# Performance work log

Measured on AMD Instinct MI355X. Metric: run time of the kernel, lower is better.

The kernel has to match this reference:

```python
import jax, jax.numpy as jnp
from jax import lax
import numpy as np

H, W = 240, 304
IN_CH, OUT_CH, K = 16, 32, 3
B = 8
N_PER = 65536
N = B * N_PER
CIN = IN_CH + 2  # pos + neg + features


def setup_inputs() -> dict:
    key = jax.random.key(0)
    k1, k2, k3, k4, k5 = jax.random.split(key, 5)
    # events columns: x, y, t in [0,1); polarity in {0,1}
    xyt = jax.random.uniform(k1, (N, 3), dtype=jnp.float32)
    pol = jax.random.randint(k2, (N, 1), 0, 2).astype(jnp.float32)
    events = jnp.concatenate([xyt, pol], axis=1)
    features = jax.random.normal(k3, (N, IN_CH), dtype=jnp.float32)
    offsets = (jnp.arange(1, B + 1, dtype=jnp.int64) * N_PER)  # cumulative counts
    # SubmanifoldConvolution params: one [CIN, OUT_CH] matrix per filter offset -> HWIO
    fan_in = K * K * CIN
    weight = jax.random.normal(k4, (K, K, CIN, OUT_CH), dtype=jnp.float32) / np.sqrt(fan_in)
    bias = jax.random.normal(k5, (OUT_CH,), dtype=jnp.float32) * 0.01
    return {"events": events, "features": features, "weight": weight,
            "bias": bias, "offsets": offsets}


def reference(events, features, weight, bias, offsets):
    n = events.shape[0]
    b = offsets.shape[0]
    # offset2batch: row i belongs to first sample whose cumulative offset exceeds i
    batch = jnp.searchsorted(offsets, jnp.arange(n, dtype=offsets.dtype), side="right").astype(jnp.int32)
    pos = events[:, 3:4]
    neg = 1.0 - pos
    sparse = jnp.concatenate([pos, neg, features], axis=1)  # [N, CIN]
    # yx = events[:, [1, 0]] scaled by (h, w), rounded to grid coords
    yi = jnp.clip(jnp.round(events[:, 1] * H).astype(jnp.int32), 0, H - 1)
    xi = jnp.clip(jnp.round(events[:, 0] * W).astype(jnp.int32), 0, W - 1)
    key = (batch * H + yi) * W + xi  # linear site id, [N]
    nseg = b * H * W
    # scn InputLayer mode=4: average features of duplicate coordinates
    feat_sum = jax.ops.segment_sum(sparse, key, num_segments=nseg)  # [nseg, CIN]
    cnt = jax.ops.segment_sum(jnp.ones((n,), sparse.dtype), key, num_segments=nseg)
    dense = feat_sum / jnp.maximum(cnt, 1.0)[:, None]
    dense = dense.reshape(b, H, W, CIN)  # zeros at inactive sites
    # Submanifold 3x3 conv: inactive neighbors are zero, so a dense SAME conv
    # evaluated only at active sites matches the submanifold rulebook math.
    out = lax.conv_general_dilated(dense, weight, window_strides=(1, 1),
                                   padding="SAME",
                                   dimension_numbers=("NHWC", "HWIO", "NHWC"))
    out = out.reshape(nseg, OUT_CH)
    # OutputLayer: read back per input row (active sites only), add bias there
    f = out[key] + bias  # [N, OUT_CH]
    return f
```

## Files before the change

kernel.cpp:

```cpp
#include <hip/hip_runtime.h>

#define Hh 240
#define Ww 304
#define IN_CH 16
#define OUT_CH 32
#define Bb 8
#define N_PER 65536
#define N_EV (Bb * N_PER)
#define CIN (IN_CH + 2)
#define NSEG (Bb * Hh * Ww)
#define NBLK 570

#define TW 32
#define TH 8
#define HW_ 34
#define HH_ 10
#define NXT_TILES 10
#define NYT_TILES 30
#define OPITCH 33

typedef __attribute__((ext_vector_type(8))) short bf16x8;
typedef __attribute__((ext_vector_type(4))) float f32x4;

__device__ __forceinline__ unsigned short f2bf(float x) {
  unsigned u = __float_as_uint(x);
  unsigned r = u + 0x7fffu + ((u >> 16) & 1u);
  return (unsigned short)(r >> 16);
}
__device__ __forceinline__ float bf2f(unsigned short b) {
  return __uint_as_float(((unsigned)b) << 16);
}

__global__ __launch_bounds__(256) void hist_rank_kernel(
    const float* __restrict__ events, const int* __restrict__ offsets,
    int* __restrict__ hist, int* __restrict__ keyArr, int* __restrict__ rankArr) {
  int i = blockIdx.x * blockDim.x + threadIdx.x;
  float4 ev = ((const float4*)events)[i];
  int yi = (int)rintf(ev.y * (float)Hh);
  yi = min(max(yi, 0), Hh - 1);
  int xi = (int)rintf(ev.x * (float)Ww);
  xi = min(max(xi, 0), Ww - 1);
  int b = 0;
#pragma unroll
  for (int j = 0; j < Bb; j++) b += (offsets[j] <= i) ? 1 : 0;
  int key = (b * Hh + yi) * Ww + xi;
  int pol = (ev.w != 0.0f) ? 1 : 0;
  keyArr[i] = key | (pol << 31);
  rankArr[i] = atomicAdd(&hist[key], 1);
}

__global__ __launch_bounds__(256) void scan1_kernel(
    const int* __restrict__ hist, int* __restrict__ baseLocal,
    int* __restrict__ blockSum) {
  __shared__ int lds[256];
  int b = blockIdx.x, t = threadIdx.x;
  int idx = b * 1024 + t * 4;
  int4 v = *(const int4*)(hist + idx);
  int s0 = v.x, s1 = s0 + v.y, s2 = s1 + v.z, s3 = s2 + v.w;
  lds[t] = s3;
  __syncthreads();
  int val = s3;
  for (int off = 1; off < 256; off <<= 1) {
    int n = (t >= off) ? lds[t - off] : 0;
    __syncthreads();
    val += n;
    lds[t] = val;
    __syncthreads();
  }
  int excl = val - s3;
  int4 o;
  o.x = excl; o.y = excl + s0; o.z = excl + s1; o.w = excl + s2;
  *(int4*)(baseLocal + idx) = o;
  if (t == 255) blockSum[b] = val;
}

__global__ __launch_bounds__(1024) void scan2_kernel(
    const int* __restrict__ blockSum, int* __restrict__ blockOffset) {
  __shared__ int lds[1024];
  int t = threadIdx.x;
  int v = (t < NBLK) ? blockSum[t] : 0;
  lds[t] = v;
  __syncthreads();
  int val = v;
  for (int off = 1; off < 1024; off <<= 1) {
    int n = (t >= off) ? lds[t - off] : 0;
    __syncthreads();
    val += n;
    lds[t] = val;
    __syncthreads();
  }
  if (t < NBLK) blockOffset[t] = val - v;
  if (t == 0) blockOffset[NBLK] = lds[1023];
}

__global__ __launch_bounds__(256) void prep_weights_kernel(
    const float* __restrict__ weight, unsigned short* __restrict__ wprep) {
  int tid = threadIdx.x;
#pragma unroll
  for (int it = 0; it < 24; it++) {
    int idx = it * 256 + tid;
    int ky = idx >> 11;
    int rem = idx & 2047;
    int n = rem >> 6;
    int kl = rem & 63;
    unsigned short v = 0;
    if (kl < 54) {
      int kx = kl / 18, ci = kl - kx * 18;
      v = f2bf(weight[((ky * 3 + kx) * CIN + ci) * OUT_CH + n]);
    }
    wprep[idx] = v;
  }
}

__global__ __launch_bounds__(256) void scatter_feat_kernel(
    const float* __restrict__ features, const int* __restrict__ keyArr,
    const int* __restrict__ rankArr, const int* __restrict__ baseLocal,
    const int* __restrict__ blockOffset, uint4* __restrict__ sortedFeat,
    int* __restrict__ sortedMeta) {
  int i = blockIdx.x * blockDim.x + threadIdx.x;
  int meta = keyArr[i];
  int key = meta & 0x7fffffff;
  int pos = baseLocal[key] + blockOffset[key >> 10] + rankArr[i];
  const float4* f = (const float4*)(features + (size_t)i * IN_CH);
  float4 f0 = f[0], f1 = f[1], f2 = f[2], f3 = f[3];
  uint4 w0, w1;
  w0.x = (unsigned)f2bf(f0.x) | ((unsigned)f2bf(f0.y) << 16);
  w0.y = (unsigned)f2bf(f0.z) | ((unsigned)f2bf(f0.w) << 16);
  w0.z = (unsigned)f2bf(f1.x) | ((unsigned)f2bf(f1.y) << 16);
  w0.w = (unsigned)f2bf(f1.z) | ((unsigned)f2bf(f1.w) << 16);
  w1.x = (unsigned)f2bf(f2.x) | ((unsigned)f2bf(f2.y) << 16);
  w1.y = (unsigned)f2bf(f2.z) | ((unsigned)f2bf(f2.w) << 16);
  w1.z = (unsigned)f2bf(f3.x) | ((unsigned)f2bf(f3.y) << 16);
  w1.w = (unsigned)f2bf(f3.z) | ((unsigned)f2bf(f3.w) << 16);
  sortedFeat[(size_t)pos * 2] = w0;
  sortedFeat[(size_t)pos * 2 + 1] = w1;
  sortedMeta[pos] = i | (meta & 0x80000000);
}

__global__ __launch_bounds__(256) void fused_conv_kernel(
    const uint4* __restrict__ sortedFeat, const int* __restrict__ sortedMeta,
    const int* __restrict__ baseLocal, const int* __restrict__ blockOffset,
    const unsigned short* __restrict__ wprep, const float* __restrict__ bias,
    float* __restrict__ out) {
  __shared__ unsigned smem[128 * OPITCH];
  __shared__ int ibase[TH * TW];
  __shared__ int icnt[TH * TW];

  int blk = blockIdx.x;
  int xt = blk % NXT_TILES;
  int rem = blk / NXT_TILES;
  int yt = rem % NYT_TILES;
  int b = rem / NYT_TILES;
  int x0 = xt * TW, y0 = yt * TH;
  int tid = threadIdx.x;

  if (tid < 12) smem[3060 + tid] = 0;

  for (int h = tid; h < HH_ * HW_; h += 256) {
    int hy = h / HW_, hx = h % HW_;
    int gy = y0 - 1 + hy, gx = x0 - 1 + hx;
    float acc[CIN];
#pragma unroll
    for (int k = 0; k < CIN; k++) acc[k] = 0.0f;
    int c = 0, base = 0;
    if (gy >= 0 && gy < Hh && gx >= 0 && gx < Ww) {
      int p = (b * Hh + gy) * Ww + gx;
      int bo = blockOffset[p >> 10];
      base = baseLocal[p] + bo;
      int nxt = ((p & 1023) != 1023) ? (baseLocal[p + 1] + bo)
                                     : blockOffset[(p >> 10) + 1];
      c = nxt - base;
      for (int j = 0; j < c; j++) {
        int e = sortedMeta[base + j];
        float pol = (float)((unsigned)e >> 31);
        acc[0] += pol;
        acc[1] += 1.0f - pol;
        uint4 w0 = sortedFeat[(size_t)(base + j) * 2];
        uint4 w1 = sortedFeat[(size_t)(base + j) * 2 + 1];
        acc[2] += bf2f((unsigned short)w0.x);  acc[3] += bf2f((unsigned short)(w0.x >> 16));
        acc[4] += bf2f((unsigned short)w0.y);  acc[5] += bf2f((unsigned short)(w0.y >> 16));
        acc[6] += bf2f((unsigned short)w0.z);  acc[7] += bf2f((unsigned short)(w0.z >> 16));
        acc[8] += bf2f((unsigned short)w0.w);  acc[9] += bf2f((unsigned short)(w0.w >> 16));
        acc[10] += bf2f((unsigned short)w1.x); acc[11] += bf2f((unsigned short)(w1.x >> 16));
        acc[12] += bf2f((unsigned short)w1.y); acc[13] += bf2f((unsigned short)(w1.y >> 16));
        acc[14] += bf2f((unsigned short)w1.z); acc[15] += bf2f((unsigned short)(w1.z >> 16));
        acc[16] += bf2f((unsigned short)w1.w); acc[17] += bf2f((unsigned short)(w1.w >> 16));
      }
    }
    float inv = 1.0f / fmaxf((float)c, 1.0f);
    unsigned* row = smem + 9 * h;
#pragma unroll
    for (int k = 0; k < 9; k++)
      row[k] = (unsigned)f2bf(acc[2 * k] * inv) |
               ((unsigned)f2bf(acc[2 * k + 1] * inv) << 16);
    if (hx >= 1 && hx <= TW && hy >= 1 && hy <= TH) {
      int t = (hy - 1) * TW + (hx - 1);
      ibase[t] = base;
      icnt[t] = c;
    }
  }
  __syncthreads();

  int wv = tid >> 6, lane = tid & 63;
  int quad = lane >> 4, lrow = lane & 15;

  f32x4 accf[4][2];
#pragma unroll
  for (int i = 0; i < 4; i++)
#pragma unroll
    for (int nt = 0; nt < 2; nt++) accf[i][nt] = (f32x4){0.f, 0.f, 0.f, 0.f};

  const unsigned* hp = smem;
#pragma unroll
  for (int ky = 0; ky < 3; ky++) {
    bf16x8 bfr[2][2];
#pragma unroll
    for (int kh = 0; kh < 2; kh++)
#pragma unroll
      for (int nt = 0; nt < 2; nt++) {
        int n = nt * 16 + lrow;
        bfr[kh][nt] = *(const bf16x8*)(wprep + ((ky * 32 + n) << 6) +
                                       kh * 32 + quad * 8);
      }
#pragma unroll
    for (int i = 0; i < 4; i++) {
      int t0 = (wv * 4 + i) * 16;
      int ox = (t0 & 31) + lrow;
      int oy = t0 >> 5;
      int idx0 = ((oy + ky) * HW_ + ox) * CIN;
#pragma unroll
      for (int kh = 0; kh < 2; kh++) {
        union { bf16x8 v; unsigned u[4]; } a;
        int ui = (idx0 >> 1) + kh * 16 + quad * 4;
        a.u[0] = hp[ui]; a.u[1] = hp[ui + 1];
        a.u[2] = hp[ui + 2]; a.u[3] = hp[ui + 3];
        accf[i][0] = __builtin_amdgcn_mfma_f32_16x16x32_bf16(
            a.v, bfr[kh][0], accf[i][0], 0, 0, 0);
        accf[i][1] = __builtin_amdgcn_mfma_f32_16x16x32_bf16(
            a.v, bfr[kh][1], accf[i][1], 0, 0, 0);
      }
    }
  }
  __syncthreads();

  float* outsh = (float*)smem;
  float bn0 = bias[lrow], bn1 = bias[16 + lrow];
  int gx = x0 + (tid & 31);
  int c = icnt[tid];
  int base = ibase[tid];
#pragma unroll
  for (int ch = 0; ch < 2; ch++) {
#pragma unroll
    for (int ii = 0; ii < 2; ii++) {
      int i = ch * 2 + ii;
      int lidx = ii * 16 + quad * 4;
      int row = wv * 32 + lidx;
#pragma unroll
      for (int r = 0; r < 4; r++) {
        outsh[(row + r) * OPITCH + lrow] = accf[i][0][r] + bn0;
        outsh[(row + r) * OPITCH + 16 + lrow] = accf[i][1][r] + bn1;
      }
    }
    __syncthreads();
    if (((tid >> 5) & 1) == ch && gx < Ww && c > 0) {
      int row = (tid >> 6) * 32 + ((tid & 63) - ch * 32);
      const float* rp = outsh + row * OPITCH;
      float4 o0 = make_float4(rp[0], rp[1], rp[2], rp[3]);
      float4 o1 = make_float4(rp[4], rp[5], rp[6], rp[7]);
      float4 o2 = make_float4(rp[8], rp[9], rp[10], rp[11]);
      float4 o3 = make_float4(rp[12], rp[13], rp[14], rp[15]);
      float4 o4 = make_float4(rp[16], rp[17], rp[18], rp[19]);
      float4 o5 = make_float4(rp[20], rp[21], rp[22], rp[23]);
      float4 o6 = make_float4(rp[24], rp[25], rp[26], rp[27]);
      float4 o7 = make_float4(rp[28], rp[29], rp[30], rp[31]);
      for (int j = 0; j < c; j++) {
        int ev = sortedMeta[base + j] & 0x7fffffff;
        float4* op = (float4*)(out + (size_t)ev * OUT_CH);
        op[0] = o0; op[1] = o1; op[2] = o2; op[3] = o3;
        op[4] = o4; op[5] = o5; op[6] = o6; op[7] = o7;
      }
    }
    __syncthreads();
  }
}

extern "C" void kernel_launch(void* const* d_in, const int* in_sizes, int n_in,
                              void* d_out, int out_size, void* d_ws,
                              size_t ws_size, hipStream_t stream) {
  const float* events = (const float*)d_in[0];
  const float* features = (const float*)d_in[1];
  const float* weight = (const float*)d_in[2];
  const float* bias = (const float*)d_in[3];
  const int* offsets = (const int*)d_in[4];
  float* out = (float*)d_out;

  uint4* sortedFeat = (uint4*)d_ws;
  int* sortedMeta = (int*)(sortedFeat + (size_t)N_EV * 2);
  int* keyArr = sortedMeta + N_EV;
  int* rankArr = keyArr + N_EV;
  int* hist = rankArr + N_EV;
  int* baseLocal = hist + NSEG;
  int* blockOffset = baseLocal + NSEG;
  int* blockSum = blockOffset + 1024;
  unsigned short* wprep = (unsigned short*)(blockSum + 1024);

  hipMemsetAsync(hist, 0, (size_t)NSEG * sizeof(int), stream);

  hist_rank_kernel<<<N_EV / 256, 256, 0, stream>>>(events, offsets, hist,
                                                   keyArr, rankArr);
  prep_weights_kernel<<<1, 256, 0, stream>>>(weight, wprep);
  scan1_kernel<<<NBLK, 256, 0, stream>>>(hist, baseLocal, blockSum);
  scan2_kernel<<<1, 1024, 0, stream>>>(blockSum, blockOffset);
  scatter_feat_kernel<<<N_EV / 256, 256, 0, stream>>>(
      features, keyArr, rankArr, baseLocal, blockOffset, sortedFeat, sortedMeta);
  fused_conv_kernel<<<Bb * NYT_TILES * NXT_TILES, 256, 0, stream>>>(
      sortedFeat, sortedMeta, baseLocal, blockOffset, wprep, bias, out);
}
```

Before: 189.5 us.

## Merge preprocessing kernels into one cooperative kernel with grid syncs

Replaces the memset and the histogram, scan, weight-prep and scatter kernels with a single cooperative kernel that uses grid-wide barriers between phases. Each thread handles two events and keeps key, rank and packed bf16 features in registers across phases, so the keyArr/rankArr round trips through global memory and the second feature read go away. It also cuts several kernel launches and launch gaps. In exchange, the kernel now depends on 1024 blocks being co-resident and adds four grid.sync barriers, with idle blocks during the scan phases.

```diff
diff --git a/kernel.cpp b/kernel.cpp
--- a/kernel.cpp
+++ b/kernel.cpp
@@ -1,4 +1,7 @@
 #include <hip/hip_runtime.h>
+#include <hip/hip_cooperative_groups.h>
+
+namespace cg = cooperative_groups;
 
 #define Hh 240
 #define Ww 304
@@ -11,6 +14,10 @@
 #define NSEG (Bb * Hh * Ww)
 #define NBLK 570
 
+#define COOP_BLOCKS 1024
+#define COOP_THREADS 256
+#define COOP_TOTAL (COOP_BLOCKS * COOP_THREADS)
+
 #define TW 32
 #define TH 8
 #define HW_ 34
@@ -30,111 +37,121 @@
 __device__ __forceinline__ float bf2f(unsigned short b) {
   return __uint_as_float(((unsigned)b) << 16);
 }
-
-__global__ __launch_bounds__(256) void hist_rank_kernel(
-    const float* __restrict__ events, const int* __restrict__ offsets,
-    int* __restrict__ hist, int* __restrict__ keyArr, int* __restrict__ rankArr) {
-  int i = blockIdx.x * blockDim.x + threadIdx.x;
-  float4 ev = ((const float4*)events)[i];
-  int yi = (int)rintf(ev.y * (float)Hh);
-  yi = min(max(yi, 0), Hh - 1);
-  int xi = (int)rintf(ev.x * (float)Ww);
-  xi = min(max(xi, 0), Ww - 1);
-  int b = 0;
-#pragma unroll
-  for (int j = 0; j < Bb; j++) b += (offsets[j] <= i) ? 1 : 0;
-  int key = (b * Hh + yi) * Ww + xi;
-  int pol = (ev.w != 0.0f) ? 1 : 0;
-  keyArr[i] = key | (pol << 31);
-  rankArr[i] = atomicAdd(&hist[key], 1);
-}
-
-__global__ __launch_bounds__(256) void scan1_kernel(
-    const int* __restrict__ hist, int* __restrict__ baseLocal,
-    int* __restrict__ blockSum) {
+__device__ __forceinline__ unsigned pk2(float a, float b) {
+  return (unsigned)f2bf(a) | ((unsigned)f2bf(b) << 16);
+}
+
+__global__ __launch_bounds__(256, 4) void prep_kernel(
+    const float* __restrict__ events, const float* __restrict__ features,
+    const float* __restrict__ weight, const int* __restrict__ offsets,
+    int* __restrict__ hist, int* __restrict__ baseLocal,
+    int* __restrict__ blockOffset, int* __restrict__ blockSum,
+    unsigned short* __restrict__ wprep, uint4* __restrict__ sortedFeat,
+    int* __restrict__ sortedMeta) {
+  cg::grid_group grid = cg::this_grid();
   __shared__ int lds[256];
-  int b = blockIdx.x, t = threadIdx.x;
-  int idx = b * 1024 + t * 4;
-  int4 v = *(const int4*)(hist + idx);
-  int s0 = v.x, s1 = s0 + v.y, s2 = s1 + v.z, s3 = s2 + v.w;
-  lds[t] = s3;
-  __syncthreads();
-  int val = s3;
-  for (int off = 1; off < 256; off <<= 1) {
-    int n = (t >= off) ? lds[t - off] : 0;
+  int tid = threadIdx.x;
+  int gtid = blockIdx.x * COOP_THREADS + tid;
+
+  for (int i = gtid; i < NSEG / 4; i += COOP_TOTAL)
+    ((int4*)hist)[i] = make_int4(0, 0, 0, 0);
+  grid.sync();
+
+  int key[2], rank[2];
+  uint4 w0[2], w1[2];
+#pragma unroll
+  for (int s = 0; s < 2; s++) {
+    int i = gtid + s * COOP_TOTAL;
+    float4 ev = ((const float4*)events)[i];
+    int yi = min(max((int)rintf(ev.y * (float)Hh), 0), Hh - 1);
+    int xi = min(max((int)rintf(ev.x * (float)Ww), 0), Ww - 1);
+    int b = 0;
+#pragma unroll
+    for (int j = 0; j < Bb; j++) b += (offsets[j] <= i) ? 1 : 0;
+    int k = (b * Hh + yi) * Ww + xi;
+    rank[s] = atomicAdd(&hist[k], 1);
+    key[s] = k | ((ev.w != 0.0f) ? (int)0x80000000 : 0);
+    const float4* f = (const float4*)(features + (size_t)i * IN_CH);
+    float4 f0 = f[0], f1 = f[1], f2 = f[2], f3 = f[3];
+    w0[s].x = pk2(f0.x, f0.y); w0[s].y = pk2(f0.z, f0.w);
+    w0[s].z = pk2(f1.x, f1.y); w0[s].w = pk2(f1.z, f1.w);
+    w1[s].x = pk2(f2.x, f2.y); w1[s].y = pk2(f2.z, f2.w);
+    w1[s].z = pk2(f3.x, f3.y); w1[s].w = pk2(f3.z, f3.w);
+  }
+  grid.sync();
+
+  if (blockIdx.x < NBLK) {
+    int idx = blockIdx.x * 1024 + tid * 4;
+    int4 v = *(const int4*)(hist + idx);
+    int s0 = v.x, s1 = s0 + v.y, s2 = s1 + v.z, s3 = s2 + v.w;
+    lds[tid] = s3;
     __syncthreads();
-    val += n;
-    lds[t] = val;
+    int val = s3;
+    for (int off = 1; off < 256; off <<= 1) {
+      int n = (tid >= off) ? lds[tid - off] : 0;
+      __syncthreads();
+      val += n;
+      lds[tid] = val;
+      __syncthreads();
+    }
+    int excl = val - s3;
+    int4 o;
+    o.x = excl; o.y = excl + s0; o.z = excl + s1; o.w = excl + s2;
+    *(int4*)(baseLocal + idx) = o;
+    if (tid == 255) blockSum[blockIdx.x] = val;
+  } else if (blockIdx.x == NBLK) {
+#pragma unroll
+    for (int it = 0; it < 24; it++) {
+      int idx = it * 256 + tid;
+      int ky = idx >> 11;
+      int rem = idx & 2047;
+      int n = rem >> 6;
+      int kl = rem & 63;
+      unsigned short v = 0;
+      if (kl < 54) {
+        int kx = kl / 18, ci = kl - kx * 18;
+        v = f2bf(weight[((ky * 3 + kx) * CIN + ci) * OUT_CH + n]);
+      }
+      wprep[idx] = v;
+    }
+  }
+  grid.sync();
+
+  if (blockIdx.x == 0) {
+    int idx = tid * 4;
+    int a0 = (idx + 0 < NBLK) ? blockSum[idx + 0] : 0;
+    int a1 = (idx + 1 < NBLK) ? blockSum[idx + 1] : 0;
+    int a2 = (idx + 2 < NBLK) ? blockSum[idx + 2] : 0;
+    int a3 = (idx + 3 < NBLK) ? blockSum[idx + 3] : 0;
+    int s0 = a0, s1 = s0 + a1, s2 = s1 + a2, s3 = s2 + a3;
+    lds[tid] = s3;
     __syncthreads();
-  }
-  int excl = val - s3;
-  int4 o;
-  o.x = excl; o.y = excl + s0; o.z = excl + s1; o.w = excl + s2;
-  *(int4*)(baseLocal + idx) = o;
-  if (t == 255) blockSum[b] = val;
-}
-
-__global__ __launch_bounds__(1024) void scan2_kernel(
-    const int* __restrict__ blockSum, int* __restrict__ blockOffset) {
-  __shared__ int lds[1024];
-  int t = threadIdx.x;
-  int v = (t < NBLK) ? blockSum[t] : 0;
-  lds[t] = v;
-  __syncthreads();
-  int val = v;
-  for (int off = 1; off < 1024; off <<= 1) {
-    int n = (t >= off) ? lds[t - off] : 0;
-    __syncthreads();
-    val += n;
-    lds[t] = val;
-    __syncthreads();
-  }
-  if (t < NBLK) blockOffset[t] = val - v;
-  if (t == 0) blockOffset[NBLK] = lds[1023];
-}
-
-__global__ __launch_bounds__(256) void prep_weights_kernel(
-    const float* __restrict__ weight, unsigned short* __restrict__ wprep) {
-  int tid = threadIdx.x;
-#pragma unroll
-  for (int it = 0; it < 24; it++) {
-    int idx = it * 256 + tid;
-    int ky = idx >> 11;
-    int rem = idx & 2047;
-    int n = rem >> 6;
-    int kl = rem & 63;
-    unsigned short v = 0;
-    if (kl < 54) {
-      int kx = kl / 18, ci = kl - kx * 18;
-      v = f2bf(weight[((ky * 3 + kx) * CIN + ci) * OUT_CH + n]);
-    }
-    wprep[idx] = v;
-  }
-}
-
-__global__ __launch_bounds__(256) void scatter_feat_kernel(
-    const float* __restrict__ features, const int* __restrict__ keyArr,
-    const int* __restrict__ rankArr, const int* __restrict__ baseLocal,
-    const int* __restrict__ blockOffset, uint4* __restrict__ sortedFeat,
-    int* __restrict__ sortedMeta) {
-  int i = blockIdx.x * blockDim.x + threadIdx.x;
-  int meta = keyArr[i];
-  int key = meta & 0x7fffffff;
-  int pos = baseLocal[key] + blockOffset[key >> 10] + rankArr[i];
-  const float4* f = (const float4*)(features + (size_t)i * IN_CH);
-  float4 f0 = f[0], f1 = f[1], f2 = f[2], f3 = f[3];
-  uint4 w0, w1;
-  w0.x = (unsigned)f2bf(f0.x) | ((unsigned)f2bf(f0.y) << 16);
-  w0.y = (unsigned)f2bf(f0.z) | ((unsigned)f2bf(f0.w) << 16);
-  w0.z = (unsigned)f2bf(f1.x) | ((unsigned)f2bf(f1.y) << 16);
-  w0.w = (unsigned)f2bf(f1.z) | ((unsigned)f2bf(f1.w) << 16);
-  w1.x = (unsigned)f2bf(f2.x) | ((unsigned)f2bf(f2.y) << 16);
-  w1.y = (unsigned)f2bf(f2.z) | ((unsigned)f2bf(f2.w) << 16);
-  w1.z = (unsigned)f2bf(f3.x) | ((unsigned)f2bf(f3.y) << 16);
-  w1.w = (unsigned)f2bf(f3.z) | ((unsigned)f2bf(f3.w) << 16);
-  sortedFeat[(size_t)pos * 2] = w0;
-  sortedFeat[(size_t)pos * 2 + 1] = w1;
-  sortedMeta[pos] = i | (meta & 0x80000000);
+    int val = s3;
+    for (int off = 1; off < 256; off <<= 1) {
+      int n = (tid >= off) ? lds[tid - off] : 0;
+      __syncthreads();
+      val += n;
+      lds[tid] = val;
+      __syncthreads();
+    }
+    int excl = val - s3;
+    if (idx + 0 < NBLK) blockOffset[idx + 0] = excl;
+    if (idx + 1 < NBLK) blockOffset[idx + 1] = excl + s0;
+    if (idx + 2 < NBLK) blockOffset[idx + 2] = excl + s1;
+    if (idx + 3 < NBLK) blockOffset[idx + 3] = excl + s2;
+    if (tid == 255) blockOffset[NBLK] = val;
+  }
+  grid.sync();
+
+#pragma unroll
+  for (int s = 0; s < 2; s++) {
+    int k = key[s] & 0x7fffffff;
+    int pos = baseLocal[k] + blockOffset[k >> 10] + rank[s];
+    sortedFeat[(size_t)pos * 2] = w0[s];
+    sortedFeat[(size_t)pos * 2 + 1] = w1[s];
+    int i = gtid + s * COOP_TOTAL;
+    sortedMeta[pos] = i | (key[s] & (int)0x80000000);
+  }
 }
 
 __global__ __launch_bounds__(256) void fused_conv_kernel(
@@ -296,23 +313,18 @@
 
   uint4* sortedFeat = (uint4*)d_ws;
   int* sortedMeta = (int*)(sortedFeat + (size_t)N_EV * 2);
-  int* keyArr = sortedMeta + N_EV;
-  int* rankArr = keyArr + N_EV;
-  int* hist = rankArr + N_EV;
+  int* hist = sortedMeta + N_EV;
   int* baseLocal = hist + NSEG;
   int* blockOffset = baseLocal + NSEG;
   int* blockSum = blockOffset + 1024;
   unsigned short* wprep = (unsigned short*)(blockSum + 1024);
 
-  hipMemsetAsync(hist, 0, (size_t)NSEG * sizeof(int), stream);
-
-  hist_rank_kernel<<<N_EV / 256, 256, 0, stream>>>(events, offsets, hist,
-                                                   keyArr, rankArr);
-  prep_weights_kernel<<<1, 256, 0, stream>>>(weight, wprep);
-  scan1_kernel<<<NBLK, 256, 0, stream>>>(hist, baseLocal, blockSum);
-  scan2_kernel<<<1, 1024, 0, stream>>>(blockSum, blockOffset);
-  scatter_feat_kernel<<<N_EV / 256, 256, 0, stream>>>(
-      features, keyArr, rankArr, baseLocal, blockOffset, sortedFeat, sortedMeta);
+  void* args[] = {(void*)&events,   (void*)&features, (void*)&weight,
+                  (void*)&offsets,  (void*)&hist,     (void*)&baseLocal,
+                  (void*)&blockOffset, (void*)&blockSum, (void*)&wprep,
+                  (void*)&sortedFeat, (void*)&sortedMeta};
+  hipLaunchCooperativeKernel((const void*)prep_kernel, dim3(COOP_BLOCKS),
+                             dim3(COOP_THREADS), args, 0, stream);
   fused_conv_kernel<<<Bb * NYT_TILES * NXT_TILES, 256, 0, stream>>>(
       sortedFeat, sortedMeta, baseLocal, blockOffset, wprep, bias, out);
 }
```

New measurement: 546.0 us. 188% more time.

## Fuse scan stages and weight prep into one kernel via atomic block offsets

Applied to the files above, without the earlier changes.

Replaces the two-pass scan (per-block scan plus single-block scan of block sums) with one kernel. Each block takes its global offset from an atomic cursor, so segment blocks are laid out in arbitrary order, and a per-block end array handles the boundary case. Weight preparation moves into an extra block of the same kernel. This removes two kernel launches and their serialization, at the cost of a nondeterministic order of the sorted event buffer across blocks.

```diff
diff --git a/kernel.cpp b/kernel.cpp
--- a/kernel.cpp
+++ b/kernel.cpp
@@ -49,11 +49,30 @@
   rankArr[i] = atomicAdd(&hist[key], 1);
 }
 
-__global__ __launch_bounds__(256) void scan1_kernel(
+__global__ __launch_bounds__(256) void scan_fused_kernel(
     const int* __restrict__ hist, int* __restrict__ baseLocal,
-    int* __restrict__ blockSum) {
+    int* __restrict__ blockOffset, int* __restrict__ blockEnd,
+    int* __restrict__ cursor, const float* __restrict__ weight,
+    unsigned short* __restrict__ wprep) {
+  int b = blockIdx.x, t = threadIdx.x;
+  if (b == NBLK) {
+#pragma unroll
+    for (int it = 0; it < 24; it++) {
+      int idx = it * 256 + t;
+      int ky = idx >> 11;
+      int rem = idx & 2047;
+      int n = rem >> 6;
+      int kl = rem & 63;
+      unsigned short v = 0;
+      if (kl < 54) {
+        int kx = kl / 18, ci = kl - kx * 18;
+        v = f2bf(weight[((ky * 3 + kx) * CIN + ci) * OUT_CH + n]);
+      }
+      wprep[idx] = v;
+    }
+    return;
+  }
   __shared__ int lds[256];
-  int b = blockIdx.x, t = threadIdx.x;
   int idx = b * 1024 + t * 4;
   int4 v = *(const int4*)(hist + idx);
   int s0 = v.x, s1 = s0 + v.y, s2 = s1 + v.z, s3 = s2 + v.w;
@@ -71,44 +90,10 @@
   int4 o;
   o.x = excl; o.y = excl + s0; o.z = excl + s1; o.w = excl + s2;
   *(int4*)(baseLocal + idx) = o;
-  if (t == 255) blockSum[b] = val;
-}
-
-__global__ __launch_bounds__(1024) void scan2_kernel(
-    const int* __restrict__ blockSum, int* __restrict__ blockOffset) {
-  __shared__ int lds[1024];
-  int t = threadIdx.x;
-  int v = (t < NBLK) ? blockSum[t] : 0;
-  lds[t] = v;
-  __syncthreads();
-  int val = v;
-  for (int off = 1; off < 1024; off <<= 1) {
-    int n = (t >= off) ? lds[t - off] : 0;
-    __syncthreads();
-    val += n;
-    lds[t] = val;
-    __syncthreads();
-  }
-  if (t < NBLK) blockOffset[t] = val - v;
-  if (t == 0) blockOffset[NBLK] = lds[1023];
-}
-
-__global__ __launch_bounds__(256) void prep_weights_kernel(
-    const float* __restrict__ weight, unsigned short* __restrict__ wprep) {
-  int tid = threadIdx.x;
-#pragma unroll
-  for (int it = 0; it < 24; it++) {
-    int idx = it * 256 + tid;
-    int ky = idx >> 11;
-    int rem = idx & 2047;
-    int n = rem >> 6;
-    int kl = rem & 63;
-    unsigned short v = 0;
-    if (kl < 54) {
-      int kx = kl / 18, ci = kl - kx * 18;
-      v = f2bf(weight[((ky * 3 + kx) * CIN + ci) * OUT_CH + n]);
-    }
-    wprep[idx] = v;
+  if (t == 255) {
+    int start = atomicAdd(cursor, val);
+    blockOffset[b] = start;
+    blockEnd[b] = start + val;
   }
 }
 
@@ -140,8 +125,8 @@
 __global__ __launch_bounds__(256) void fused_conv_kernel(
     const uint4* __restrict__ sortedFeat, const int* __restrict__ sortedMeta,
     const int* __restrict__ baseLocal, const int* __restrict__ blockOffset,
-    const unsigned short* __restrict__ wprep, const float* __restrict__ bias,
-    float* __restrict__ out) {
+    const int* __restrict__ blockEnd, const unsigned short* __restrict__ wprep,
+    const float* __restrict__ bias, float* __restrict__ out) {
   __shared__ unsigned smem[128 * OPITCH];
   __shared__ int ibase[TH * TW];
   __shared__ int icnt[TH * TW];
@@ -168,7 +153,7 @@
       int bo = blockOffset[p >> 10];
       base = baseLocal[p] + bo;
       int nxt = ((p & 1023) != 1023) ? (baseLocal[p + 1] + bo)
-                                     : blockOffset[(p >> 10) + 1];
+                                     : blockEnd[p >> 10];
       c = nxt - base;
       for (int j = 0; j < c; j++) {
         int e = sortedMeta[base + j];
@@ -299,20 +284,21 @@
   int* keyArr = sortedMeta + N_EV;
   int* rankArr = keyArr + N_EV;
   int* hist = rankArr + N_EV;
-  int* baseLocal = hist + NSEG;
+  int* cursor = hist + NSEG;
+  int* baseLocal = cursor + 4;
   int* blockOffset = baseLocal + NSEG;
-  int* blockSum = blockOffset + 1024;
-  unsigned short* wprep = (unsigned short*)(blockSum + 1024);
-
-  hipMemsetAsync(hist, 0, (size_t)NSEG * sizeof(int), stream);
+  int* blockEnd = blockOffset + 1024;
+  unsigned short* wprep = (unsigned short*)(blockEnd + 1024);
+
+  hipMemsetAsync(hist, 0, (size_t)(NSEG + 4) * sizeof(int), stream);
 
   hist_rank_kernel<<<N_EV / 256, 256, 0, stream>>>(events, offsets, hist,
                                                    keyArr, rankArr);
-  prep_weights_kernel<<<1, 256, 0, stream>>>(weight, wprep);
-  scan1_kernel<<<NBLK, 256, 0, stream>>>(hist, baseLocal, blockSum);
-  scan2_kernel<<<1, 1024, 0, stream>>>(blockSum, blockOffset);
+  scan_fused_kernel<<<NBLK + 1, 256, 0, stream>>>(
+      hist, baseLocal, blockOffset, blockEnd, cursor, weight, wprep);
   scatter_feat_kernel<<<N_EV / 256, 256, 0, stream>>>(
       features, keyArr, rankArr, baseLocal, blockOffset, sortedFeat, sortedMeta);
   fused_conv_kernel<<<Bb * NYT_TILES * NXT_TILES, 256, 0, stream>>>(
-      sortedFeat, sortedMeta, baseLocal, blockOffset, wprep, bias, out);
-}
+      sortedFeat, sortedMeta, baseLocal, blockOffset, blockEnd, wprep, bias,
+      out);
+}
```

Result: no change. 192.0 us (+1.3%).
